# Kernel optimization log

Hardware: AMD Instinct MI355X
Metric: run time of the kernel (lower is better)

## Reference

```python
import jax, jax.numpy as jnp
import numpy as np

NUM_QUBITS = 10
DIM = 2 ** NUM_QUBITS
BATCH = 16384
TWO_PI = 2.0 * np.pi


def _diag_kron(p0, p1):
    # Kronecker product of per-qubit diagonals diag(e^{i p0_k}, e^{i p1_k});
    # only the diagonal vector (length 2^n) is needed since K.dot(x, diag(d)) == x * d.
    v = jnp.stack([jnp.exp(1j * p0.astype(jnp.complex64)),
                   jnp.exp(1j * p1.astype(jnp.complex64))], axis=1)  # (n, 2)
    d = v[0]
    for k in range(1, v.shape[0]):
        d = jnp.kron(d, v[k])
    return d  # (2^n,) complex64


def _bs_kron(n):
    inv_sqrt2 = 1.0 / np.sqrt(2.0)
    bs2 = jnp.array([[1.0, 1.0j], [1.0j, 1.0]], dtype=jnp.complex64) * inv_sqrt2
    bs = bs2
    for _ in range(n - 1):
        bs = jnp.kron(bs, bs2)
    return bs  # (2^n, 2^n)


def setup_inputs() -> dict:
    key = jax.random.key(0)
    kx, ka, kb, kt, kp = jax.random.split(key, 5)
    x = jax.random.normal(kx, (BATCH, 2, DIM), dtype=jnp.float32)
    alphas = jax.random.uniform(ka, (NUM_QUBITS,), dtype=jnp.float32) * TWO_PI
    betas = jax.random.uniform(kb, (NUM_QUBITS,), dtype=jnp.float32) * TWO_PI
    thetas = jax.random.uniform(kt, (NUM_QUBITS,), dtype=jnp.float32) * TWO_PI
    phis = jax.random.uniform(kp, (NUM_QUBITS,), dtype=jnp.float32) * TWO_PI
    return {"x": x, "alphas": alphas, "betas": betas, "thetas": thetas, "phis": phis}


def reference(x, alphas, betas, thetas, phis):
    zeros = jnp.zeros_like(thetas)
    d_in = _diag_kron(alphas, betas)      # input_shifts diagonal
    d_theta = _diag_kron(thetas, zeros)   # theta_shifts diagonal
    d_phi = _diag_kron(phis, zeros)       # phi_shifts diagonal
    bs = _bs_kron(alphas.shape[0])        # dense Kronecker beamsplitter

    z = jax.lax.complex(x[:, 0], x[:, 1])  # (B, D) complex64
    z = (z * d_in) @ bs
    z = (z * d_theta) @ bs
    z = z * d_phi
    return jnp.stack([jnp.real(z), jnp.imag(z)], axis=1)  # (B, 2, D) float32
```

## Files before the change

kernel.cpp:

```cpp
#include <hip/hip_runtime.h>
#include <math.h>

#define NQ   10
#define DIMQ 1024
#define BATCH_ROWS 16384

typedef unsigned uv2 __attribute__((ext_vector_type(2)));
typedef float f32x2 __attribute__((ext_vector_type(2)));
typedef float f32x4 __attribute__((ext_vector_type(4)));

#if __has_builtin(__builtin_amdgcn_permlane32_swap)
#define HAS_PLS32 1
#else
#define HAS_PLS32 0
#endif
#if __has_builtin(__builtin_amdgcn_permlane16_swap)
#define HAS_PLS16 1
#else
#define HAS_PLS16 0
#endif

__device__ __forceinline__ float2 cmulc(float2 a, float2 b) {
    return make_float2(a.x * b.x - a.y * b.y, a.x * b.y + a.y * b.x);
}

__global__ void qmat_precompute(const float* __restrict__ alphas,
                                const float* __restrict__ betas,
                                const float* __restrict__ thetas,
                                const float* __restrict__ phis,
                                float* __restrict__ M) {
    const int b = threadIdx.x;
    if (b >= NQ) return;
    const int q = NQ - 1 - b;
    float sa, ca, sb, cb, st, ct, sp, cp;
    sincosf(alphas[q], &sa, &ca);
    sincosf(betas[q],  &sb, &cb);
    sincosf(thetas[q], &st, &ct);
    sincosf(phis[q],   &sp, &cp);
    const float2 u = make_float2(ca, sa), v = make_float2(cb, sb), p = make_float2(cp, sp);
    const float2 tm1  = make_float2(ct - 1.f, st);
    const float2 itp1 = make_float2(-st, ct + 1.f);
    const float2 omt  = make_float2(1.f - ct, -st);
    float2 m00 = cmulc(cmulc(p, u), tm1);
    float2 m01 = cmulc(cmulc(p, v), itp1);
    float2 m10 = cmulc(u, itp1);
    float2 m11 = cmulc(v, omt);
    const float s = 0.5f;
    M[b * 8 + 0] = m00.x * s; M[b * 8 + 1] = m00.y * s;
    M[b * 8 + 2] = m01.x * s; M[b * 8 + 3] = m01.y * s;
    M[b * 8 + 4] = m10.x * s; M[b * 8 + 5] = m10.y * s;
    M[b * 8 + 6] = m11.x * s; M[b * 8 + 7] = m11.y * s;
}

template <int CTRL>
__device__ __forceinline__ float dpp_mov(float x) {
    return __int_as_float(
        __builtin_amdgcn_update_dpp(0, __float_as_int(x), CTRL, 0xF, 0xF, true));
}
template <int PAT>
__device__ __forceinline__ float ds_swz(float x) {
    return __int_as_float(__builtin_amdgcn_ds_swizzle(__float_as_int(x), PAT));
}
template <int CTRL>
__device__ __forceinline__ f32x2 pk_dpp(f32x2 v) {
    return (f32x2){dpp_mov<CTRL>(v.x), dpp_mov<CTRL>(v.y)};
}
template <int PAT>
__device__ __forceinline__ f32x2 pk_swz(f32x2 v) {
    return (f32x2){ds_swz<PAT>(v.x), ds_swz<PAT>(v.y)};
}
__device__ __forceinline__ f32x2 pk_shfl_xor(f32x2 v, int m) {
    return (f32x2){__shfl_xor(v.x, m, 64), __shfl_xor(v.y, m, 64)};
}
__device__ __forceinline__ f32x2 pk_swap(f32x2 v) { return (f32x2){v.y, v.x}; }

#define DPP_XOR1 0xB1
#define DPP_XOR2 0x4E
#define SWZ_XOR4 0x101F
#define SWZ_XOR8 0x201F

__device__ __forceinline__ int orient_pls32(unsigned lane) {
#if HAS_PLS32
    uv2 r = __builtin_amdgcn_permlane32_swap(lane, 1000u + lane, false, false);
    const bool lo = lane < 32;
    unsigned ax = lo ? lane : (1000u + lane - 32u);
    unsigned ay = lo ? (lane + 32u) : (1000u + lane);
    unsigned bx = lo ? (1000u + lane + 32u) : lane;
    unsigned by = lo ? (1000u + lane) : (lane - 32u);
    if (__all(r.x == ax && r.y == ay)) return 2;
    if (__all(r.x == bx && r.y == by)) return 1;
#endif
    return 0;
}
__device__ __forceinline__ int orient_pls16(unsigned lane) {
#if HAS_PLS16
    uv2 r = __builtin_amdgcn_permlane16_swap(lane, 1000u + lane, false, false);
    const bool hi = (lane & 16u) != 0u;
    unsigned ax = hi ? (1000u + lane - 16u) : lane;
    unsigned ay = hi ? (1000u + lane) : (lane + 16u);
    unsigned bx = hi ? lane : (1000u + lane + 16u);
    unsigned by = hi ? (lane - 16u) : (1000u + lane);
    if (__all(r.x == ax && r.y == ay)) return 2;
    if (__all(r.x == bx && r.y == by)) return 1;
#endif
    return 0;
}

__device__ __forceinline__ void pk_mstage(f32x2& ar, f32x2& ai, f32x2& br, f32x2& bi,
                                          float m0, float m1, float m2, float m3,
                                          float m4, float m5, float m6, float m7) {
    f32x2 nar = m0 * ar - m1 * ai + m2 * br - m3 * bi;
    f32x2 nai = m0 * ai + m1 * ar + m2 * bi + m3 * br;
    f32x2 nbr = m4 * ar - m5 * ai + m6 * br - m7 * bi;
    f32x2 nbi = m4 * ai + m5 * ar + m6 * bi + m7 * br;
    ar = nar; ai = nai; br = nbr; bi = nbi;
}

template <class F>
__device__ __forceinline__ void pk_fetch_stage(f32x2 re[2][4], f32x2 im[2][4],
                                               float c0r, float c0i, float c1r, float c1i,
                                               F fetch) {
#pragma unroll
    for (int p = 0; p < 2; ++p)
#pragma unroll
        for (int l = 0; l < 4; ++l) {
            const f32x2 r = re[p][l], i = im[p][l];
            const f32x2 pr = fetch(r), pi = fetch(i);
            re[p][l] = c0r * r - c0i * i + c1r * pr - c1i * pi;
            im[p][l] = c0r * i + c0i * r + c1r * pi + c1i * pr;
        }
}

#if HAS_PLS32
__device__ __forceinline__ void pk_pls32_mstage(f32x2& fr, f32x2& fi, f32x2& gr, f32x2& gi,
                                                float m0, float m1, float m2, float m3,
                                                float m4, float m5, float m6, float m7,
                                                bool orientA) {
    uv2 rx = __builtin_amdgcn_permlane32_swap(__float_as_uint(fr.x), __float_as_uint(gr.x), false, false);
    uv2 ry = __builtin_amdgcn_permlane32_swap(__float_as_uint(fr.y), __float_as_uint(gr.y), false, false);
    uv2 ix = __builtin_amdgcn_permlane32_swap(__float_as_uint(fi.x), __float_as_uint(gi.x), false, false);
    uv2 iy = __builtin_amdgcn_permlane32_swap(__float_as_uint(fi.y), __float_as_uint(gi.y), false, false);
    f32x2 pxr = {__uint_as_float(rx.x), __uint_as_float(ry.x)};
    f32x2 pyr = {__uint_as_float(rx.y), __uint_as_float(ry.y)};
    f32x2 pxi = {__uint_as_float(ix.x), __uint_as_float(iy.x)};
    f32x2 pyi = {__uint_as_float(ix.y), __uint_as_float(iy.y)};
    f32x2 A1r, A1i, A2r, A2i;
    if (orientA) {
        A1r = m0 * pxr - m1 * pxi + m2 * pyr - m3 * pyi;
        A1i = m0 * pxi + m1 * pxr + m2 * pyi + m3 * pyr;
        A2r = m4 * pxr - m5 * pxi + m6 * pyr - m7 * pyi;
        A2i = m4 * pxi + m5 * pxr + m6 * pyi + m7 * pyr;
    } else {
        A1r = m6 * pxr - m7 * pxi + m4 * pyr - m5 * pyi;
        A1i = m6 * pxi + m7 * pxr + m4 * pyi + m5 * pyr;
        A2r = m2 * pxr - m3 * pxi + m0 * pyr - m1 * pyi;
        A2i = m2 * pxi + m3 * pxr + m0 * pyi + m1 * pyr;
    }
    uv2 ox = __builtin_amdgcn_permlane32_swap(__float_as_uint(A1r.x), __float_as_uint(A2r.x), false, false);
    uv2 oy = __builtin_amdgcn_permlane32_swap(__float_as_uint(A1r.y), __float_as_uint(A2r.y), false, false);
    uv2 px = __builtin_amdgcn_permlane32_swap(__float_as_uint(A1i.x), __float_as_uint(A2i.x), false, false);
    uv2 py = __builtin_amdgcn_permlane32_swap(__float_as_uint(A1i.y), __float_as_uint(A2i.y), false, false);
    fr = (f32x2){__uint_as_float(ox.x), __uint_as_float(oy.x)};
    gr = (f32x2){__uint_as_float(ox.y), __uint_as_float(oy.y)};
    fi = (f32x2){__uint_as_float(px.x), __uint_as_float(py.x)};
    gi = (f32x2){__uint_as_float(px.y), __uint_as_float(py.y)};
}
#endif
#if HAS_PLS16
__device__ __forceinline__ void pk_pls16_mstage(f32x2& fr, f32x2& fi, f32x2& gr, f32x2& gi,
                                                float m0, float m1, float m2, float m3,
                                                float m4, float m5, float m6, float m7,
                                                bool orientA) {
    uv2 rx = __builtin_amdgcn_permlane16_swap(__float_as_uint(fr.x), __float_as_uint(gr.x), false, false);
    uv2 ry = __builtin_amdgcn_permlane16_swap(__float_as_uint(fr.y), __float_as_uint(gr.y), false, false);
    uv2 ix = __builtin_amdgcn_permlane16_swap(__float_as_uint(fi.x), __float_as_uint(gi.x), false, false);
    uv2 iy = __builtin_amdgcn_permlane16_swap(__float_as_uint(fi.y), __float_as_uint(gi.y), false, false);
    f32x2 pxr = {__uint_as_float(rx.x), __uint_as_float(ry.x)};
    f32x2 pyr = {__uint_as_float(rx.y), __uint_as_float(ry.y)};
    f32x2 pxi = {__uint_as_float(ix.x), __uint_as_float(iy.x)};
    f32x2 pyi = {__uint_as_float(ix.y), __uint_as_float(iy.y)};
    f32x2 A1r, A1i, A2r, A2i;
    if (orientA) {
        A1r = m0 * pxr - m1 * pxi + m2 * pyr - m3 * pyi;
        A1i = m0 * pxi + m1 * pxr + m2 * pyi + m3 * pyr;
        A2r = m4 * pxr - m5 * pxi + m6 * pyr - m7 * pyi;
        A2i = m4 * pxi + m5 * pxr + m6 * pyi + m7 * pyr;
    } else {
        A1r = m6 * pxr - m7 * pxi + m4 * pyr - m5 * pyi;
        A1i = m6 * pxi + m7 * pxr + m4 * pyi + m5 * pyr;
        A2r = m2 * pxr - m3 * pxi + m0 * pyr - m1 * pyi;
        A2i = m2 * pxi + m3 * pxr + m0 * pyi + m1 * pyr;
    }
    uv2 ox = __builtin_amdgcn_permlane16_swap(__float_as_uint(A1r.x), __float_as_uint(A2r.x), false, false);
    uv2 oy = __builtin_amdgcn_permlane16_swap(__float_as_uint(A1r.y), __float_as_uint(A2r.y), false, false);
    uv2 px = __builtin_amdgcn_permlane16_swap(__float_as_uint(A1i.x), __float_as_uint(A2i.x), false, false);
    uv2 py = __builtin_amdgcn_permlane16_swap(__float_as_uint(A1i.y), __float_as_uint(A2i.y), false, false);
    fr = (f32x2){__uint_as_float(ox.x), __uint_as_float(oy.x)};
    gr = (f32x2){__uint_as_float(ox.y), __uint_as_float(oy.y)};
    fi = (f32x2){__uint_as_float(px.x), __uint_as_float(py.x)};
    gi = (f32x2){__uint_as_float(px.y), __uint_as_float(py.y)};
}
#endif

template <bool USE_WS>
__global__ __launch_bounds__(256)
void qlayer_fused(const float* __restrict__ x, const float* __restrict__ Mtab,
                  const float* __restrict__ alphas, const float* __restrict__ betas,
                  const float* __restrict__ thetas, const float* __restrict__ phis,
                  float* __restrict__ out) {
    const int lane = threadIdx.x & 63;
    const int wv   = threadIdx.x >> 6;
    const int row  = blockIdx.x * 4 + wv;

    const int o16 = orient_pls16((unsigned)lane);
    const int o32 = orient_pls32((unsigned)lane);

    const float* __restrict__ xr = x + (size_t)row * (2 * DIMQ);
    float* __restrict__ orow     = out + (size_t)row * (2 * DIMQ);

    float Ml[NQ * 8];
    if (!USE_WS) {
#pragma unroll
        for (int b = 0; b < NQ; ++b) {
            const int q = NQ - 1 - b;
            float sa, ca, sb, cb, st, ct, sp, cp;
            sincosf(alphas[q], &sa, &ca);
            sincosf(betas[q],  &sb, &cb);
            sincosf(thetas[q], &st, &ct);
            sincosf(phis[q],   &sp, &cp);
            const float2 u = make_float2(ca, sa), v = make_float2(cb, sb), p2 = make_float2(cp, sp);
            const float2 tm1  = make_float2(ct - 1.f, st);
            const float2 itp1 = make_float2(-st, ct + 1.f);
            const float2 omt  = make_float2(1.f - ct, -st);
            float2 m00 = cmulc(cmulc(p2, u), tm1);
            float2 m01 = cmulc(cmulc(p2, v), itp1);
            float2 m10 = cmulc(u, itp1);
            float2 m11 = cmulc(v, omt);
            Ml[b * 8 + 0] = m00.x * .5f; Ml[b * 8 + 1] = m00.y * .5f;
            Ml[b * 8 + 2] = m01.x * .5f; Ml[b * 8 + 3] = m01.y * .5f;
            Ml[b * 8 + 4] = m10.x * .5f; Ml[b * 8 + 5] = m10.y * .5f;
            Ml[b * 8 + 6] = m11.x * .5f; Ml[b * 8 + 7] = m11.y * .5f;
        }
    }

    f32x2 Pre[2][4], Pim[2][4];
#pragma unroll
    for (int p = 0; p < 2; ++p) {
        const f32x4 rA = *(const f32x4*)(xr + (2 * p + 0) * 256 + lane * 4);
        const f32x4 iA = *(const f32x4*)(xr + DIMQ + (2 * p + 0) * 256 + lane * 4);
        const f32x4 rB = *(const f32x4*)(xr + (2 * p + 1) * 256 + lane * 4);
        const f32x4 iB = *(const f32x4*)(xr + DIMQ + (2 * p + 1) * 256 + lane * 4);
#pragma unroll
        for (int l = 0; l < 4; ++l) {
            Pre[p][l] = (f32x2){rA[l], rB[l]};
            Pim[p][l] = (f32x2){iA[l], iB[l]};
        }
    }

    float m0, m1, m2, m3, m4, m5, m6, m7;
#define LOADM(s_) do {                                                     \
    if (USE_WS) {                                                          \
        m0 = Mtab[(s_) * 8 + 0]; m1 = Mtab[(s_) * 8 + 1];                  \
        m2 = Mtab[(s_) * 8 + 2]; m3 = Mtab[(s_) * 8 + 3];                  \
        m4 = Mtab[(s_) * 8 + 4]; m5 = Mtab[(s_) * 8 + 5];                  \
        m6 = Mtab[(s_) * 8 + 6]; m7 = Mtab[(s_) * 8 + 7];                  \
    } else {                                                               \
        m0 = Ml[(s_) * 8 + 0]; m1 = Ml[(s_) * 8 + 1];                      \
        m2 = Ml[(s_) * 8 + 2]; m3 = Ml[(s_) * 8 + 3];                      \
        m4 = Ml[(s_) * 8 + 4]; m5 = Ml[(s_) * 8 + 5];                      \
        m6 = Ml[(s_) * 8 + 6]; m7 = Ml[(s_) * 8 + 7];                      \
    }                                                                      \
} while (0)
#define SELC(maskbit) \
    const bool hb = (lane & (maskbit)) != 0;                               \
    const float c0r = hb ? m6 : m0, c0i = hb ? m7 : m1;                    \
    const float c1r = hb ? m4 : m2, c1i = hb ? m5 : m3;

    LOADM(0);
#pragma unroll
    for (int p = 0; p < 2; ++p) {
        pk_mstage(Pre[p][0], Pim[p][0], Pre[p][1], Pim[p][1], m0, m1, m2, m3, m4, m5, m6, m7);
        pk_mstage(Pre[p][2], Pim[p][2], Pre[p][3], Pim[p][3], m0, m1, m2, m3, m4, m5, m6, m7);
    }
    LOADM(1);
#pragma unroll
    for (int p = 0; p < 2; ++p) {
        pk_mstage(Pre[p][0], Pim[p][0], Pre[p][2], Pim[p][2], m0, m1, m2, m3, m4, m5, m6, m7);
        pk_mstage(Pre[p][1], Pim[p][1], Pre[p][3], Pim[p][3], m0, m1, m2, m3, m4, m5, m6, m7);
    }
    {
        LOADM(2);
        SELC(1);
        pk_fetch_stage(Pre, Pim, c0r, c0i, c1r, c1i,
                       [](f32x2 v) { return pk_dpp<DPP_XOR1>(v); });
    }
    {
        LOADM(3);
        SELC(2);
        pk_fetch_stage(Pre, Pim, c0r, c0i, c1r, c1i,
                       [](f32x2 v) { return pk_dpp<DPP_XOR2>(v); });
    }
    {
        LOADM(4);
        SELC(4);
        pk_fetch_stage(Pre, Pim, c0r, c0i, c1r, c1i,
                       [](f32x2 v) { return pk_swz<SWZ_XOR4>(v); });
    }
    {
        LOADM(5);
        SELC(8);
        pk_fetch_stage(Pre, Pim, c0r, c0i, c1r, c1i,
                       [](f32x2 v) { return pk_swz<SWZ_XOR8>(v); });
    }
    {
        LOADM(6);
#if HAS_PLS16
        if (o16 != 0) {
            const bool oA = (o16 == 2);
#pragma unroll
            for (int p = 0; p < 2; ++p) {
                pk_pls16_mstage(Pre[p][0], Pim[p][0], Pre[p][1], Pim[p][1], m0, m1, m2, m3, m4, m5, m6, m7, oA);
                pk_pls16_mstage(Pre[p][2], Pim[p][2], Pre[p][3], Pim[p][3], m0, m1, m2, m3, m4, m5, m6, m7, oA);
            }
        } else
#endif
        {
            SELC(16);
            pk_fetch_stage(Pre, Pim, c0r, c0i, c1r, c1i,
                           [](f32x2 v) { return pk_shfl_xor(v, 16); });
        }
    }
    {
        LOADM(7);
#if HAS_PLS32
        if (o32 != 0) {
            const bool oA = (o32 == 2);
#pragma unroll
            for (int p = 0; p < 2; ++p) {
                pk_pls32_mstage(Pre[p][0], Pim[p][0], Pre[p][1], Pim[p][1], m0, m1, m2, m3, m4, m5, m6, m7, oA);
                pk_pls32_mstage(Pre[p][2], Pim[p][2], Pre[p][3], Pim[p][3], m0, m1, m2, m3, m4, m5, m6, m7, oA);
            }
        } else
#endif
        {
            SELC(32);
            pk_fetch_stage(Pre, Pim, c0r, c0i, c1r, c1i,
                           [](f32x2 v) { return pk_shfl_xor(v, 32); });
        }
    }
    {
        LOADM(8);
        const f32x2 csr = {m0, m6}, csi = {m1, m7};
        const f32x2 cor = {m2, m4}, coi = {m3, m5};
#pragma unroll
        for (int p = 0; p < 2; ++p)
#pragma unroll
            for (int l = 0; l < 4; ++l) {
                const f32x2 r = Pre[p][l], i = Pim[p][l];
                const f32x2 Sr = pk_swap(r), Si = pk_swap(i);
                Pre[p][l] = csr * r - csi * i + cor * Sr - coi * Si;
                Pim[p][l] = csr * i + csi * r + cor * Si + coi * Sr;
            }
    }
    LOADM(9);
#pragma unroll
    for (int l = 0; l < 4; ++l)
        pk_mstage(Pre[0][l], Pim[0][l], Pre[1][l], Pim[1][l], m0, m1, m2, m3, m4, m5, m6, m7);
#undef LOADM
#undef SELC

#pragma unroll
    for (int p = 0; p < 2; ++p)
#pragma unroll
        for (int c = 0; c < 2; ++c) {
            const int j = 2 * p + c;
            f32x4 r4 = {Pre[p][0][c], Pre[p][1][c], Pre[p][2][c], Pre[p][3][c]};
            f32x4 i4 = {Pim[p][0][c], Pim[p][1][c], Pim[p][2][c], Pim[p][3][c]};
            __builtin_nontemporal_store(r4, (f32x4*)(orow + j * 256 + lane * 4));
            __builtin_nontemporal_store(i4, (f32x4*)(orow + DIMQ + j * 256 + lane * 4));
        }
}

extern "C" void kernel_launch(void* const* d_in, const int* in_sizes, int n_in,
                              void* d_out, int out_size, void* d_ws, size_t ws_size,
                              hipStream_t stream) {
    const float* x      = (const float*)d_in[0];
    const float* alphas = (const float*)d_in[1];
    const float* betas  = (const float*)d_in[2];
    const float* thetas = (const float*)d_in[3];
    const float* phis   = (const float*)d_in[4];
    float* out = (float*)d_out;

    const int blocks = BATCH_ROWS / 4;

    if (ws_size >= NQ * 8 * sizeof(float)) {
        float* M = (float*)d_ws;
        qmat_precompute<<<1, 64, 0, stream>>>(alphas, betas, thetas, phis, M);
        qlayer_fused<true><<<blocks, 256, 0, stream>>>(x, M, alphas, betas, thetas, phis, out);
    } else {
        qlayer_fused<false><<<blocks, 256, 0, stream>>>(x, nullptr, alphas, betas, thetas, phis, out);
    }
}
```

Measured before the change: 54.23 us.

## Process two rows per wavefront and prefetch the second row during compute

```diff
diff --git a/kernel.cpp b/kernel.cpp
--- a/kernel.cpp
+++ b/kernel.cpp
@@ -202,21 +202,170 @@
 }
 #endif
 
+__device__ __forceinline__ void load_raw(const float* __restrict__ xr, int lane,
+                                         f32x4 raw[2][4]) {
+#pragma unroll
+    for (int p = 0; p < 2; ++p) {
+        raw[p][0] = *(const f32x4*)(xr + (2 * p + 0) * 256 + lane * 4);
+        raw[p][1] = *(const f32x4*)(xr + DIMQ + (2 * p + 0) * 256 + lane * 4);
+        raw[p][2] = *(const f32x4*)(xr + (2 * p + 1) * 256 + lane * 4);
+        raw[p][3] = *(const f32x4*)(xr + DIMQ + (2 * p + 1) * 256 + lane * 4);
+    }
+}
+
+__device__ __forceinline__ void pack_raw(const f32x4 raw[2][4],
+                                         f32x2 Pre[2][4], f32x2 Pim[2][4]) {
+#pragma unroll
+    for (int p = 0; p < 2; ++p)
+#pragma unroll
+        for (int l = 0; l < 4; ++l) {
+            Pre[p][l] = (f32x2){raw[p][0][l], raw[p][2][l]};
+            Pim[p][l] = (f32x2){raw[p][1][l], raw[p][3][l]};
+        }
+}
+
+__device__ __forceinline__ void store_state(float* __restrict__ orow, int lane,
+                                            const f32x2 Pre[2][4], const f32x2 Pim[2][4]) {
+#pragma unroll
+    for (int p = 0; p < 2; ++p)
+#pragma unroll
+        for (int c = 0; c < 2; ++c) {
+            const int j = 2 * p + c;
+            f32x4 r4 = {Pre[p][0][c], Pre[p][1][c], Pre[p][2][c], Pre[p][3][c]};
+            f32x4 i4 = {Pim[p][0][c], Pim[p][1][c], Pim[p][2][c], Pim[p][3][c]};
+            __builtin_nontemporal_store(r4, (f32x4*)(orow + j * 256 + lane * 4));
+            __builtin_nontemporal_store(i4, (f32x4*)(orow + DIMQ + j * 256 + lane * 4));
+        }
+}
+
 template <bool USE_WS>
-__global__ __launch_bounds__(256)
+__device__ __forceinline__ void apply_stages(f32x2 Pre[2][4], f32x2 Pim[2][4],
+                                             const float* __restrict__ Mtab,
+                                             const float* __restrict__ Ml,
+                                             int lane, int o16, int o32) {
+    float m0, m1, m2, m3, m4, m5, m6, m7;
+#define LOADM(s_) do {                                                     \
+    const float* _mp = USE_WS ? (Mtab + (s_) * 8) : (Ml + (s_) * 8);       \
+    m0 = _mp[0]; m1 = _mp[1]; m2 = _mp[2]; m3 = _mp[3];                    \
+    m4 = _mp[4]; m5 = _mp[5]; m6 = _mp[6]; m7 = _mp[7];                    \
+} while (0)
+#define SELC(maskbit) \
+    const bool hb = (lane & (maskbit)) != 0;                               \
+    const float c0r = hb ? m6 : m0, c0i = hb ? m7 : m1;                    \
+    const float c1r = hb ? m4 : m2, c1i = hb ? m5 : m3;
+
+    LOADM(0);
+#pragma unroll
+    for (int p = 0; p < 2; ++p) {
+        pk_mstage(Pre[p][0], Pim[p][0], Pre[p][1], Pim[p][1], m0, m1, m2, m3, m4, m5, m6, m7);
+        pk_mstage(Pre[p][2], Pim[p][2], Pre[p][3], Pim[p][3], m0, m1, m2, m3, m4, m5, m6, m7);
+    }
+    LOADM(1);
+#pragma unroll
+    for (int p = 0; p < 2; ++p) {
+        pk_mstage(Pre[p][0], Pim[p][0], Pre[p][2], Pim[p][2], m0, m1, m2, m3, m4, m5, m6, m7);
+        pk_mstage(Pre[p][1], Pim[p][1], Pre[p][3], Pim[p][3], m0, m1, m2, m3, m4, m5, m6, m7);
+    }
+    {
+        LOADM(2);
+        SELC(1);
+        pk_fetch_stage(Pre, Pim, c0r, c0i, c1r, c1i,
+                       [](f32x2 v) { return pk_dpp<DPP_XOR1>(v); });
+    }
+    {
+        LOADM(3);
+        SELC(2);
+        pk_fetch_stage(Pre, Pim, c0r, c0i, c1r, c1i,
+                       [](f32x2 v) { return pk_dpp<DPP_XOR2>(v); });
+    }
+    {
+        LOADM(4);
+        SELC(4);
+        pk_fetch_stage(Pre, Pim, c0r, c0i, c1r, c1i,
+                       [](f32x2 v) { return pk_swz<SWZ_XOR4>(v); });
+    }
+    {
+        LOADM(5);
+        SELC(8);
+        pk_fetch_stage(Pre, Pim, c0r, c0i, c1r, c1i,
+                       [](f32x2 v) { return pk_swz<SWZ_XOR8>(v); });
+    }
+    {
+        LOADM(6);
+#if HAS_PLS16
+        if (o16 != 0) {
+            const bool oA = (o16 == 2);
+#pragma unroll
+            for (int p = 0; p < 2; ++p) {
+                pk_pls16_mstage(Pre[p][0], Pim[p][0], Pre[p][1], Pim[p][1], m0, m1, m2, m3, m4, m5, m6, m7, oA);
+                pk_pls16_mstage(Pre[p][2], Pim[p][2], Pre[p][3], Pim[p][3], m0, m1, m2, m3, m4, m5, m6, m7, oA);
+            }
+        } else
+#endif
+        {
+            SELC(16);
+            pk_fetch_stage(Pre, Pim, c0r, c0i, c1r, c1i,
+                           [](f32x2 v) { return pk_shfl_xor(v, 16); });
+        }
+    }
+    {
+        LOADM(7);
+#if HAS_PLS32
+        if (o32 != 0) {
+            const bool oA = (o32 == 2);
+#pragma unroll
+            for (int p = 0; p < 2; ++p) {
+                pk_pls32_mstage(Pre[p][0], Pim[p][0], Pre[p][1], Pim[p][1], m0, m1, m2, m3, m4, m5, m6, m7, oA);
+                pk_pls32_mstage(Pre[p][2], Pim[p][2], Pre[p][3], Pim[p][3], m0, m1, m2, m3, m4, m5, m6, m7, oA);
+            }
+        } else
+#endif
+        {
+            SELC(32);
+            pk_fetch_stage(Pre, Pim, c0r, c0i, c1r, c1i,
+                           [](f32x2 v) { return pk_shfl_xor(v, 32); });
+        }
+    }
+    {
+        LOADM(8);
+        const f32x2 csr = {m0, m6}, csi = {m1, m7};
+        const f32x2 cor = {m2, m4}, coi = {m3, m5};
+#pragma unroll
+        for (int p = 0; p < 2; ++p)
+#pragma unroll
+            for (int l = 0; l < 4; ++l) {
+                const f32x2 r = Pre[p][l], i = Pim[p][l];
+                const f32x2 Sr = pk_swap(r), Si = pk_swap(i);
+                Pre[p][l] = csr * r - csi * i + cor * Sr - coi * Si;
+                Pim[p][l] = csr * i + csi * r + cor * Si + coi * Sr;
+            }
+    }
+    LOADM(9);
+#pragma unroll
+    for (int l = 0; l < 4; ++l)
+        pk_mstage(Pre[0][l], Pim[0][l], Pre[1][l], Pim[1][l], m0, m1, m2, m3, m4, m5, m6, m7);
+#undef LOADM
+#undef SELC
+}
+
+template <bool USE_WS>
+__global__ __launch_bounds__(256, 6)
 void qlayer_fused(const float* __restrict__ x, const float* __restrict__ Mtab,
                   const float* __restrict__ alphas, const float* __restrict__ betas,
                   const float* __restrict__ thetas, const float* __restrict__ phis,
                   float* __restrict__ out) {
     const int lane = threadIdx.x & 63;
     const int wv   = threadIdx.x >> 6;
-    const int row  = blockIdx.x * 4 + wv;
+    const int gw   = blockIdx.x * 4 + wv;
+    const int row0 = gw * 2;
 
     const int o16 = orient_pls16((unsigned)lane);
     const int o32 = orient_pls32((unsigned)lane);
 
-    const float* __restrict__ xr = x + (size_t)row * (2 * DIMQ);
-    float* __restrict__ orow     = out + (size_t)row * (2 * DIMQ);
+    const float* __restrict__ xr0 = x + (size_t)row0 * (2 * DIMQ);
+    const float* __restrict__ xr1 = xr0 + 2 * DIMQ;
+    float* __restrict__ or0       = out + (size_t)row0 * (2 * DIMQ);
+    float* __restrict__ or1       = or0 + 2 * DIMQ;
 
     float Ml[NQ * 8];
     if (!USE_WS) {
@@ -243,142 +392,20 @@
         }
     }
 
+    f32x4 raw0[2][4];
+    load_raw(xr0, lane, raw0);
     f32x2 Pre[2][4], Pim[2][4];
-#pragma unroll
-    for (int p = 0; p < 2; ++p) {
-        const f32x4 rA = *(const f32x4*)(xr + (2 * p + 0) * 256 + lane * 4);
-        const f32x4 iA = *(const f32x4*)(xr + DIMQ + (2 * p + 0) * 256 + lane * 4);
-        const f32x4 rB = *(const f32x4*)(xr + (2 * p + 1) * 256 + lane * 4);
-        const f32x4 iB = *(const f32x4*)(xr + DIMQ + (2 * p + 1) * 256 + lane * 4);
-#pragma unroll
-        for (int l = 0; l < 4; ++l) {
-            Pre[p][l] = (f32x2){rA[l], rB[l]};
-            Pim[p][l] = (f32x2){iA[l], iB[l]};
-        }
-    }
-
-    float m0, m1, m2, m3, m4, m5, m6, m7;
-#define LOADM(s_) do {                                                     \
-    if (USE_WS) {                                                          \
-        m0 = Mtab[(s_) * 8 + 0]; m1 = Mtab[(s_) * 8 + 1];                  \
-        m2 = Mtab[(s_) * 8 + 2]; m3 = Mtab[(s_) * 8 + 3];                  \
-        m4 = Mtab[(s_) * 8 + 4]; m5 = Mtab[(s_) * 8 + 5];                  \
-        m6 = Mtab[(s_) * 8 + 6]; m7 = Mtab[(s_) * 8 + 7];                  \
-    } else {                                                               \
-        m0 = Ml[(s_) * 8 + 0]; m1 = Ml[(s_) * 8 + 1];                      \
-        m2 = Ml[(s_) * 8 + 2]; m3 = Ml[(s_) * 8 + 3];                      \
-        m4 = Ml[(s_) * 8 + 4]; m5 = Ml[(s_) * 8 + 5];                      \
-        m6 = Ml[(s_) * 8 + 6]; m7 = Ml[(s_) * 8 + 7];                      \
-    }                                                                      \
-} while (0)
-#define SELC(maskbit) \
-    const bool hb = (lane & (maskbit)) != 0;                               \
-    const float c0r = hb ? m6 : m0, c0i = hb ? m7 : m1;                    \
-    const float c1r = hb ? m4 : m2, c1i = hb ? m5 : m3;
-
-    LOADM(0);
-#pragma unroll
-    for (int p = 0; p < 2; ++p) {
-        pk_mstage(Pre[p][0], Pim[p][0], Pre[p][1], Pim[p][1], m0, m1, m2, m3, m4, m5, m6, m7);
-        pk_mstage(Pre[p][2], Pim[p][2], Pre[p][3], Pim[p][3], m0, m1, m2, m3, m4, m5, m6, m7);
-    }
-    LOADM(1);
-#pragma unroll
-    for (int p = 0; p < 2; ++p) {
-        pk_mstage(Pre[p][0], Pim[p][0], Pre[p][2], Pim[p][2], m0, m1, m2, m3, m4, m5, m6, m7);
-        pk_mstage(Pre[p][1], Pim[p][1], Pre[p][3], Pim[p][3], m0, m1, m2, m3, m4, m5, m6, m7);
-    }
-    {
-        LOADM(2);
-        SELC(1);
-        pk_fetch_stage(Pre, Pim, c0r, c0i, c1r, c1i,
-                       [](f32x2 v) { return pk_dpp<DPP_XOR1>(v); });
-    }
-    {
-        LOADM(3);
-        SELC(2);
-        pk_fetch_stage(Pre, Pim, c0r, c0i, c1r, c1i,
-                       [](f32x2 v) { return pk_dpp<DPP_XOR2>(v); });
-    }
-    {
-        LOADM(4);
-        SELC(4);
-        pk_fetch_stage(Pre, Pim, c0r, c0i, c1r, c1i,
-                       [](f32x2 v) { return pk_swz<SWZ_XOR4>(v); });
-    }
-    {
-        LOADM(5);
-        SELC(8);
-        pk_fetch_stage(Pre, Pim, c0r, c0i, c1r, c1i,
-                       [](f32x2 v) { return pk_swz<SWZ_XOR8>(v); });
-    }
-    {
-        LOADM(6);
-#if HAS_PLS16
-        if (o16 != 0) {
-            const bool oA = (o16 == 2);
-#pragma unroll
-            for (int p = 0; p < 2; ++p) {
-                pk_pls16_mstage(Pre[p][0], Pim[p][0], Pre[p][1], Pim[p][1], m0, m1, m2, m3, m4, m5, m6, m7, oA);
-                pk_pls16_mstage(Pre[p][2], Pim[p][2], Pre[p][3], Pim[p][3], m0, m1, m2, m3, m4, m5, m6, m7, oA);
-            }
-        } else
-#endif
-        {
-            SELC(16);
-            pk_fetch_stage(Pre, Pim, c0r, c0i, c1r, c1i,
-                           [](f32x2 v) { return pk_shfl_xor(v, 16); });
-        }
-    }
-    {
-        LOADM(7);
-#if HAS_PLS32
-        if (o32 != 0) {
-            const bool oA = (o32 == 2);
-#pragma unroll
-            for (int p = 0; p < 2; ++p) {
-                pk_pls32_mstage(Pre[p][0], Pim[p][0], Pre[p][1], Pim[p][1], m0, m1, m2, m3, m4, m5, m6, m7, oA);
-                pk_pls32_mstage(Pre[p][2], Pim[p][2], Pre[p][3], Pim[p][3], m0, m1, m2, m3, m4, m5, m6, m7, oA);
-            }
-        } else
-#endif
-        {
-            SELC(32);
-            pk_fetch_stage(Pre, Pim, c0r, c0i, c1r, c1i,
-                           [](f32x2 v) { return pk_shfl_xor(v, 32); });
-        }
-    }
-    {
-        LOADM(8);
-        const f32x2 csr = {m0, m6}, csi = {m1, m7};
-        const f32x2 cor = {m2, m4}, coi = {m3, m5};
-#pragma unroll
-        for (int p = 0; p < 2; ++p)
-#pragma unroll
-            for (int l = 0; l < 4; ++l) {
-                const f32x2 r = Pre[p][l], i = Pim[p][l];
-                const f32x2 Sr = pk_swap(r), Si = pk_swap(i);
-                Pre[p][l] = csr * r - csi * i + cor * Sr - coi * Si;
-                Pim[p][l] = csr * i + csi * r + cor * Si + coi * Sr;
-            }
-    }
-    LOADM(9);
-#pragma unroll
-    for (int l = 0; l < 4; ++l)
-        pk_mstage(Pre[0][l], Pim[0][l], Pre[1][l], Pim[1][l], m0, m1, m2, m3, m4, m5, m6, m7);
-#undef LOADM
-#undef SELC
-
-#pragma unroll
-    for (int p = 0; p < 2; ++p)
-#pragma unroll
-        for (int c = 0; c < 2; ++c) {
-            const int j = 2 * p + c;
-            f32x4 r4 = {Pre[p][0][c], Pre[p][1][c], Pre[p][2][c], Pre[p][3][c]};
-            f32x4 i4 = {Pim[p][0][c], Pim[p][1][c], Pim[p][2][c], Pim[p][3][c]};
-            __builtin_nontemporal_store(r4, (f32x4*)(orow + j * 256 + lane * 4));
-            __builtin_nontemporal_store(i4, (f32x4*)(orow + DIMQ + j * 256 + lane * 4));
-        }
+    pack_raw(raw0, Pre, Pim);
+
+    f32x4 raw1[2][4];
+    load_raw(xr1, lane, raw1);
+
+    apply_stages<USE_WS>(Pre, Pim, Mtab, Ml, lane, o16, o32);
+    store_state(or0, lane, Pre, Pim);
+
+    pack_raw(raw1, Pre, Pim);
+    apply_stages<USE_WS>(Pre, Pim, Mtab, Ml, lane, o16, o32);
+    store_state(or1, lane, Pre, Pim);
 }
 
 extern "C" void kernel_launch(void* const* d_in, const int* in_sizes, int n_in,
@@ -391,7 +418,7 @@
     const float* phis   = (const float*)d_in[4];
     float* out = (float*)d_out;
 
-    const int blocks = BATCH_ROWS / 4;
+    const int blocks = BATCH_ROWS / 8;
 
     if (ws_size >= NQ * 8 * sizeof(float)) {
         float* M = (float*)d_ws;
```

After: 117.0 us. 2.16x slower.
